# Performance work log

Hardware: AMD Instinct MI355X
Metric: run time of the kernel (lower is better)

Reference implementation:

```python
import jax, jax.numpy as jnp
import numpy as np
import math

N, D, F = 8192, 512, 2048
M, K = 4096, 128  # masked cells, masked genes per cell
EPS = 1e-5


def setup_inputs() -> dict:
    key = jax.random.key(0)
    ks = jax.random.split(key, 16)
    s = 0.02
    x = jax.random.normal(ks[0], (N, D), jnp.float32)
    # distinct masked cell indices (torch.randperm semantics)
    mask_nodes = jax.random.permutation(ks[1], N)[:M].astype(jnp.int64)
    # per-row distinct gene indices (torch.randperm per row)
    gene_idx = jnp.argsort(jax.random.uniform(ks[2], (M, D)), axis=1)[:, :K].astype(jnp.int64)
    return {
        'x': x, 'mask_nodes': mask_nodes, 'gene_idx': gene_idx,
        'Wq_e': s * jax.random.normal(ks[3], (D, D), jnp.float32),
        'Wk_e': s * jax.random.normal(ks[4], (D, D), jnp.float32),
        'Wv_e': s * jax.random.normal(ks[5], (D, D), jnp.float32),
        'ln1_g': jnp.ones((D,), jnp.float32), 'ln1_b': jnp.zeros((D,), jnp.float32),
        'ff_W1': s * jax.random.normal(ks[6], (D, F), jnp.float32),
        'ff_b1': jnp.zeros((F,), jnp.float32),
        'ff_W2': s * jax.random.normal(ks[7], (F, D), jnp.float32),
        'ff_b2': jnp.zeros((D,), jnp.float32),
        'ln2_g': jnp.ones((D,), jnp.float32), 'ln2_b': jnp.zeros((D,), jnp.float32),
        'Wq_d': s * jax.random.normal(ks[8], (D, D), jnp.float32),
        'Wk_d': s * jax.random.normal(ks[9], (D, D), jnp.float32),
        'Wv_d': s * jax.random.normal(ks[10], (D, D), jnp.float32),
        'ln3_g': jnp.ones((D,), jnp.float32), 'ln3_b': jnp.zeros((D,), jnp.float32),
        'ln4_g': jnp.ones((D,), jnp.float32), 'ln4_b': jnp.zeros((D,), jnp.float32),
        'head_W': s * jax.random.normal(ks[11], (D, D), jnp.float32),
        'head_b': jnp.zeros((D,), jnp.float32),
    }


def _ln(h, g, b):
    mu = jnp.mean(h, axis=-1, keepdims=True)
    var = jnp.mean(jnp.square(h - mu), axis=-1, keepdims=True)
    return (h - mu) * jax.lax.rsqrt(var + EPS) * g + b


def _attn(h, Wq, Wk, Wv):
    Q = h @ Wq
    Kt = h @ Wk
    V = h @ Wv
    scores = (Q @ Kt.T) / math.sqrt(D)  # [N, N]
    attn = jax.nn.softmax(scores, axis=-1)
    return attn @ V, attn


def _ff(h, W1, b1, W2, b2):
    return jax.nn.gelu(h @ W1 + b1, approximate=False) @ W2 + b2


def reference(x, mask_nodes, gene_idx,
              Wq_e, Wk_e, Wv_e, ln1_g, ln1_b,
              ff_W1, ff_b1, ff_W2, ff_b2, ln2_g, ln2_b,
              Wq_d, Wk_d, Wv_d, ln3_g, ln3_b, ln4_g, ln4_b,
              head_W, head_b):
    # mask selected genes of selected cells to 0 (encoding_mask_nodes)
    rows = mask_nodes[:, None]
    use_x = x.at[rows, gene_idx].set(0.0)

    hidden, encode_weights = _attn(use_x, Wq_e, Wk_e, Wv_e)
    hidden = _ln(hidden + use_x, ln1_g, ln1_b)
    hidden = _ln(hidden + _ff(hidden, ff_W1, ff_b1, ff_W2, ff_b2), ln2_g, ln2_b)
    # NOTE: `hidden[mask_nodes][gene_mask] = 0` in the original torch code
    # writes into a copy produced by advanced indexing -> it is a no-op.

    recon, _ = _attn(hidden, Wq_d, Wk_d, Wv_d)
    recon = _ln(recon + hidden, ln3_g, ln3_b)
    # original reuses self.ff (not self.ff1) in the decoder block
    recon = _ln(recon + _ff(recon, ff_W1, ff_b1, ff_W2, ff_b2), ln4_g, ln4_b)
    h = recon @ head_W + head_b

    x_init = x[rows, gene_idx]      # [M, K]
    x_recon = h[rows, gene_idx]     # [M, K]
    return (x_init, x_recon, encode_weights, recon)
```

## Files before the change

kernel.cpp:

```cpp
#include <hip/hip_runtime.h>
#include <hip/hip_bf16.h>
#include <stdint.h>
#include <math.h>

typedef __bf16 bf16_t;
typedef __bf16 bf16x8 __attribute__((ext_vector_type(8)));
typedef __bf16 bf16x4 __attribute__((ext_vector_type(4)));
typedef float floatx4 __attribute__((ext_vector_type(4)));

#define NN 8192
#define DD 512
#define FF 2048
#define MM 4096
#define KK 128

template<typename T> struct V16;
template<> struct V16<bf16_t> { using t = bf16x8;  static const int sh = 3; };
template<> struct V16<float>  { using t = floatx4; static const int sh = 2; };

__device__ __forceinline__ void async_copy16(const void* g, void* l) {
    __builtin_amdgcn_global_load_lds(
        (const __attribute__((address_space(1))) void*)(uintptr_t)g,
        (__attribute__((address_space(3))) void*)(uint32_t)(uintptr_t)l,
        16, 0, 0);
}

template<int EPI, typename OT>
__global__ __launch_bounds__(256, 3)
void gemm_nt(const bf16_t* __restrict__ A, const bf16_t* __restrict__ B,
             OT* __restrict__ C,
             int M, int Nc, int Kd, int ldA, int ldB, int ldC,
             long partStride, float scale, const float* __restrict__ bias,
             float* __restrict__ denom)
{
    __shared__ char smem[32768];
    bf16_t* As0 = (bf16_t*)smem;
    bf16_t* As1 = As0 + 4096;
    bf16_t* Bs0 = As0 + 8192;
    bf16_t* Bs1 = As0 + 12288;

    const int tid  = threadIdx.x;
    const int lane = tid & 63;
    const int wave = tid >> 6;
    const int wm   = (wave >> 1) << 6;
    const int wn   = (wave & 1) << 6;
    const int quad = lane >> 4;
    const int l16  = lane & 15;

    const int gx   = gridDim.x;
    const int nwg  = gx * gridDim.y;
    const int orig = blockIdx.y * gx + blockIdx.x;
    const int swz  = (orig & 7) * (nwg >> 3) + (orig >> 3);
    const long bm  = (long)(swz % gx) * 128;
    const long bn  = (long)(swz / gx) * 128;

    const int  kchunk = Kd / gridDim.z;
    const long kBeg   = (long)blockIdx.z * kchunk;
    OT* __restrict__ Co = C + (long)blockIdx.z * partStride;

    const int t0 = tid, t1 = tid + 256;
    const int r0 = t0 >> 2, q0 = (t0 & 3) ^ (r0 & 3) ^ ((r0 >> 2) & 3);
    const int r1 = t1 >> 2, q1 = (t1 & 3) ^ (r1 & 3) ^ ((r1 >> 2) & 3);
    const bf16_t* pA0 = A + (bm + r0) * (long)ldA + q0 * 8 + kBeg;
    const bf16_t* pA1 = A + (bm + r1) * (long)ldA + q1 * 8 + kBeg;
    const bf16_t* pB0 = B + (bn + r0) * (long)ldB + q0 * 8 + kBeg;
    const bf16_t* pB1 = B + (bn + r1) * (long)ldB + q1 * 8 + kBeg;

    floatx4 acc[4][4] = {};

    auto stage = [&](bf16_t* Ab, bf16_t* Bb, long k0) {
        async_copy16(pA0 + k0, Ab + t0 * 8);
        async_copy16(pA1 + k0, Ab + t1 * 8);
        async_copy16(pB0 + k0, Bb + t0 * 8);
        async_copy16(pB1 + k0, Bb + t1 * 8);
    };
    const int csw = (l16 & 3) ^ (l16 >> 2);
    auto compute = [&](const bf16_t* Ab, const bf16_t* Bb) {
        bf16x8 af[4], bfr[4];
#pragma unroll
        for (int i = 0; i < 4; i++) {
            af[i]  = *(const bf16x8*)&Ab[(wm + i * 16 + l16) * 32 + (quad ^ csw) * 8];
            bfr[i] = *(const bf16x8*)&Bb[(wn + i * 16 + l16) * 32 + (quad ^ csw) * 8];
        }
#pragma unroll
        for (int mi = 0; mi < 4; mi++)
#pragma unroll
            for (int ni = 0; ni < 4; ni++)
                acc[mi][ni] = __builtin_amdgcn_mfma_f32_16x16x32_bf16(
                    af[mi], bfr[ni], acc[mi][ni], 0, 0, 0);
    };

    const int nt = kchunk >> 5;
    stage(As0, Bs0, 0);
    __syncthreads();
    long kk = 32;
    for (int t = 0; t < nt; t += 2) {
        stage(As1, Bs1, kk); kk += 32;
        compute(As0, Bs0);
        __syncthreads();
        if (t + 2 < nt) { stage(As0, Bs0, kk); kk += 32; }
        compute(As1, Bs1);
        __syncthreads();
    }

    OT* sm = (OT*)smem;
    const int g = wm >> 6;
#pragma unroll
    for (int mi = 0; mi < 4; mi++) {
        if (mi) __syncthreads();
        const long rbase = bm + wm + mi * 16 + quad * 4;
        if (EPI == 4) {
#pragma unroll
            for (int r = 0; r < 4; r++) {
                float rsum = 0.0f;
#pragma unroll
                for (int ni = 0; ni < 4; ni++) {
                    float v = __expf(acc[mi][ni][r] * scale);
                    rsum += v;
                    sm[(g * 16 + quad * 4 + r) * 128 + wn + ni * 16 + l16] = (OT)v;
                }
                rsum += __shfl_xor(rsum, 1);
                rsum += __shfl_xor(rsum, 2);
                rsum += __shfl_xor(rsum, 4);
                rsum += __shfl_xor(rsum, 8);
                if (l16 == 0) atomicAdd(denom + rbase + r, rsum);
            }
        } else {
#pragma unroll
            for (int ni = 0; ni < 4; ni++) {
                float bv = (EPI >= 2) ? bias[bn + wn + ni * 16 + l16] : 0.0f;
#pragma unroll
                for (int r = 0; r < 4; r++) {
                    float v = acc[mi][ni][r];
                    if (EPI == 1) v *= scale;
                    if (EPI >= 2) v += bv;
                    if (EPI == 3) v = 0.5f * v * (1.0f + erff(v * 0.70710678118f));
                    sm[(g * 16 + quad * 4 + r) * 128 + wn + ni * 16 + l16] = (OT)v;
                }
            }
        }
        __syncthreads();
        typedef typename V16<OT>::t VT;
        const int VSH = V16<OT>::sh;
        const int VEC = 1 << VSH;
        const int NP  = (32 * 128) / (256 * VEC);
#pragma unroll
        for (int p = 0; p < NP; p++) {
            const int vid  = p * 256 + tid;
            const int lrow = vid >> (7 - VSH);
            const int vcol = vid & ((128 >> VSH) - 1);
            const long grow = bm + (lrow >> 4) * 64 + mi * 16 + (lrow & 15);
            *(VT*)&Co[grow * (long)ldC + bn + vcol * VEC] =
                *(const VT*)&sm[lrow * 128 + vcol * VEC];
        }
    }
}

template<int EPI, typename OT>
static void launch_gemm(const bf16_t* A, const bf16_t* B, OT* C,
                        int M, int Nc, int Kd, int lda, int ldb, int ldc,
                        int splitk, long partStride, float scale,
                        const float* bias, float* denom, hipStream_t s)
{
    dim3 g(M / 128, Nc / 128, splitk);
    gemm_nt<EPI, OT><<<g, 256, 0, s>>>(A, B, C, M, Nc, Kd, lda, ldb, ldc,
                                       partStride, scale, bias, denom);
}

__global__ __launch_bounds__(256)
void transpose_f2b(const float* __restrict__ in, bf16_t* __restrict__ out,
                   int R, int C)
{
    __shared__ float tile[32][33];
    const int bx = blockIdx.x * 32;
    const int by = blockIdx.y * 32;
    const int tx = threadIdx.x, ty = threadIdx.y;
#pragma unroll
    for (int i = 0; i < 32; i += 8)
        tile[ty + i][tx] = in[(long)(by + ty + i) * C + bx + tx];
    __syncthreads();
#pragma unroll
    for (int i = 0; i < 32; i += 8)
        out[(long)(bx + ty + i) * R + by + tx] = (bf16_t)tile[tx][ty + i];
}

__global__ __launch_bounds__(256)
void transpose_b2b(const bf16_t* __restrict__ in, bf16_t* __restrict__ out,
                   int R, int C, int ldin)
{
    __shared__ bf16_t tile[32][34];
    const int bx = blockIdx.x * 32;
    const int by = blockIdx.y * 32;
    const int tx = threadIdx.x, ty = threadIdx.y;
#pragma unroll
    for (int i = 0; i < 32; i += 8)
        tile[ty + i][tx] = in[(long)(by + ty + i) * ldin + bx + tx];
    __syncthreads();
#pragma unroll
    for (int i = 0; i < 32; i += 8)
        out[(long)(bx + ty + i) * R + by + tx] = tile[tx][ty + i];
}

__global__ __launch_bounds__(256)
void encw_norm(const bf16_t* __restrict__ P, const float* __restrict__ denom,
               float* __restrict__ out)
{
    const long row = blockIdx.x;
    const float inv = 1.0f / denom[row];
    const bf16_t* p = P + row * (long)NN;
    float* q = out + row * (long)NN;
    const int tid = threadIdx.x;
#pragma unroll
    for (int i = 0; i < 4; i++) {
        const int o = (tid + i * 256) * 8;
        bf16x8 v = *(const bf16x8*)(p + o);
        float4 lo, hi;
        lo.x = (float)v[0] * inv; lo.y = (float)v[1] * inv;
        lo.z = (float)v[2] * inv; lo.w = (float)v[3] * inv;
        hi.x = (float)v[4] * inv; hi.y = (float)v[5] * inv;
        hi.z = (float)v[6] * inv; hi.w = (float)v[7] * inv;
        *(float4*)(q + o)     = lo;
        *(float4*)(q + o + 4) = hi;
    }
}

__global__ __launch_bounds__(256)
void zero_f32(float* __restrict__ p)
{
    p[blockIdx.x * 256 + threadIdx.x] = 0.0f;
}

template<int NP, bool RS, bool CB>
__global__ __launch_bounds__(64)
void add_ln_gen(const float* __restrict__ a, long pstride,
                const float* __restrict__ rs, const float* __restrict__ cb,
                const float* __restrict__ b,
                const float* __restrict__ g, const float* __restrict__ be,
                bf16_t* __restrict__ ob, float* __restrict__ of)
{
    const long row = blockIdx.x;
    const int lane = threadIdx.x;
    const long base = row * DD + lane * 8;
    const float irs = RS ? (1.0f / rs[row]) : 1.0f;
    float v[8], s = 0.0f, s2 = 0.0f;
#pragma unroll
    for (int j = 0; j < 8; j++) {
        float t = 0.0f;
#pragma unroll
        for (int p = 0; p < NP; p++) t += a[base + j + p * pstride];
        t *= irs;
        if (CB) t += cb[lane * 8 + j];
        t += b[base + j];
        v[j] = t;
        s += t; s2 += t * t;
    }
#pragma unroll
    for (int off = 32; off > 0; off >>= 1) {
        s  += __shfl_xor(s,  off);
        s2 += __shfl_xor(s2, off);
    }
    const float mu  = s * (1.0f / DD);
    const float var = s2 * (1.0f / DD) - mu * mu;
    const float inv = rsqrtf(var + 1e-5f);
    bf16x8 o;
#pragma unroll
    for (int j = 0; j < 8; j++) {
        float r = (v[j] - mu) * inv * g[lane * 8 + j] + be[lane * 8 + j];
        o[j] = (bf16_t)r;
        of[base + j] = r;
    }
    *(bf16x8*)(ob + base) = o;
}

__global__ __launch_bounds__(256)
void build_usex(const float* __restrict__ x, bf16_t* __restrict__ ub,
                float* __restrict__ uf)
{
    const long i = ((long)blockIdx.x * 256 + threadIdx.x) * 4;
    const float4 v = *(const float4*)(x + i);
    *(float4*)(uf + i) = v;
    bf16x4 o = { (bf16_t)v.x, (bf16_t)v.y, (bf16_t)v.z, (bf16_t)v.w };
    *(bf16x4*)(ub + i) = o;
}

__global__ __launch_bounds__(256)
void scatter_zero(bf16_t* __restrict__ ub, float* __restrict__ uf,
                  const int* __restrict__ mn, const int* __restrict__ gi)
{
    const int i = blockIdx.x * 256 + threadIdx.x;
    const long idx = (long)mn[i >> 7] * DD + gi[i];
    ub[idx] = (bf16_t)0.0f;
    uf[idx] = 0.0f;
}

__global__ __launch_bounds__(256)
void gather_mk(const float* __restrict__ src, const int* __restrict__ mn,
               const int* __restrict__ gi, float* __restrict__ dst)
{
    const int i = blockIdx.x * 256 + threadIdx.x;
    dst[i] = src[(long)mn[i >> 7] * DD + gi[i]];
}

__global__ __launch_bounds__(256)
void gather_head(const float* __restrict__ p1, long pstride,
                 const float* __restrict__ hb, const int* __restrict__ mn,
                 const int* __restrict__ gi, float* __restrict__ dst)
{
    const int i = blockIdx.x * 256 + threadIdx.x;
    const int col = gi[i];
    const long idx = (long)mn[i >> 7] * DD + col;
    dst[i] = p1[idx] + p1[idx + pstride] + hb[col];
}

extern "C" void kernel_launch(void* const* d_in, const int* in_sizes, int n_in,
                              void* d_out, int out_size, void* d_ws, size_t ws_size,
                              hipStream_t stream)
{
    const float* x      = (const float*)d_in[0];
    const int*   mn     = (const int*)d_in[1];
    const int*   gi     = (const int*)d_in[2];
    const float* Wq_e   = (const float*)d_in[3];
    const float* Wk_e   = (const float*)d_in[4];
    const float* Wv_e   = (const float*)d_in[5];
    const float* ln1_g  = (const float*)d_in[6];
    const float* ln1_b  = (const float*)d_in[7];
    const float* ff_W1  = (const float*)d_in[8];
    const float* ff_b1  = (const float*)d_in[9];
    const float* ff_W2  = (const float*)d_in[10];
    const float* ff_b2  = (const float*)d_in[11];
    const float* ln2_g  = (const float*)d_in[12];
    const float* ln2_b  = (const float*)d_in[13];
    const float* Wq_d   = (const float*)d_in[14];
    const float* Wk_d   = (const float*)d_in[15];
    const float* Wv_d   = (const float*)d_in[16];
    const float* ln3_g  = (const float*)d_in[17];
    const float* ln3_b  = (const float*)d_in[18];
    const float* ln4_g  = (const float*)d_in[19];
    const float* ln4_b  = (const float*)d_in[20];
    const float* head_W = (const float*)d_in[21];
    const float* head_b = (const float*)d_in[22];

    float* outf     = (float*)d_out;
    float* o_xinit  = outf;
    float* o_xrecon = outf + (size_t)MM * KK;
    float* o_encw   = outf + (size_t)2 * MM * KK;
    float* o_recon  = o_encw + (size_t)NN * NN;

    char* ws = (char*)d_ws;
    size_t off = 0;
    auto alloc = [&](size_t bytes) -> void* {
        void* p = ws + off;
        off += (bytes + 255) & ~(size_t)255;
        return p;
    };
    const size_t NDb = (size_t)NN * DD * sizeof(bf16_t);
    const size_t NDf = (size_t)NN * DD * sizeof(float);
    const long   NDe = (long)NN * DD;

    bf16_t* usex_b = (bf16_t*)alloc(NDb);
    bf16_t* qkv_b  = (bf16_t*)alloc((size_t)NN * 3 * DD * 2);
    bf16_t* vt_b   = (bf16_t*)alloc(NDb);
    bf16_t* hid_b  = (bf16_t*)alloc(NDb);
    float*  usex_f = (float*)alloc(NDf);
    float*  resA_f = (float*)alloc(NDf);
    float*  part_f = (float*)alloc(2 * NDf);
    bf16_t* wt_qe  = (bf16_t*)alloc((size_t)DD * DD * 2);
    bf16_t* wt_ke  = (bf16_t*)alloc((size_t)DD * DD * 2);
    bf16_t* wt_ve  = (bf16_t*)alloc((size_t)DD * DD * 2);
    bf16_t* wt_qd  = (bf16_t*)alloc((size_t)DD * DD * 2);
    bf16_t* wt_kd  = (bf16_t*)alloc((size_t)DD * DD * 2);
    bf16_t* wt_vd  = (bf16_t*)alloc((size_t)DD * DD * 2);
    bf16_t* wt_h   = (bf16_t*)alloc((size_t)DD * DD * 2);
    bf16_t* w1t    = (bf16_t*)alloc((size_t)DD * FF * 2);
    bf16_t* w2t    = (bf16_t*)alloc((size_t)FF * DD * 2);
    float*  denom  = (float*)alloc((size_t)NN * sizeof(float));
    bf16_t* scores = (bf16_t*)alloc((size_t)NN * NN * 2);
    bf16_t* t1_b   = scores;
    float*  resB_f = usex_f;
    (void)ws_size; (void)in_sizes; (void)n_in; (void)out_size;
    (void)wt_ke; (void)wt_ve; (void)wt_kd; (void)wt_vd;

    auto tr = [&](const float* in, bf16_t* o, int R, int C) {
        transpose_f2b<<<dim3(C / 32, R / 32), dim3(32, 8), 0, stream>>>(in, o, R, C);
    };
    const float SC = 0.04419417382f;

    tr(Wq_e, wt_qe, DD, DD);  tr(Wk_e, wt_ke, DD, DD);  tr(Wv_e, wt_ve, DD, DD);
    tr(Wq_d, wt_qd, DD, DD);  tr(Wk_d, wt_kd, DD, DD);  tr(Wv_d, wt_vd, DD, DD);
    tr(head_W, wt_h, DD, DD); tr(ff_W1, w1t, DD, FF);   tr(ff_W2, w2t, FF, DD);

    build_usex<<<NN * DD / 1024, 256, 0, stream>>>(x, usex_b, usex_f);
    scatter_zero<<<MM * KK / 256, 256, 0, stream>>>(usex_b, usex_f, mn, gi);
    gather_mk<<<MM * KK / 256, 256, 0, stream>>>(x, mn, gi, o_xinit);

    launch_gemm<0, bf16_t>(usex_b, wt_qe, qkv_b,
                           NN, 3 * DD, DD, DD, DD, 3 * DD, 1, 0, 0.f, nullptr,
                           nullptr, stream);
    transpose_b2b<<<dim3(DD / 32, NN / 32), dim3(32, 8), 0, stream>>>(
        qkv_b + 2 * DD, vt_b, NN, DD, 3 * DD);
    zero_f32<<<NN / 256, 256, 0, stream>>>(denom);
    launch_gemm<4, bf16_t>(qkv_b, qkv_b + DD, scores,
                           NN, NN, DD, 3 * DD, 3 * DD, NN, 1, 0, SC, nullptr,
                           denom, stream);
    encw_norm<<<NN, 256, 0, stream>>>(scores, denom, o_encw);
    launch_gemm<0, float>(scores, vt_b, part_f,
                          NN, DD, NN, NN, NN, DD, 2, NDe, 0.f, nullptr,
                          nullptr, stream);
    add_ln_gen<2, true, false><<<NN, 64, 0, stream>>>(
        part_f, NDe, denom, nullptr, usex_f, ln1_g, ln1_b, hid_b, resA_f);

    launch_gemm<3, bf16_t>(hid_b, w1t, t1_b,
                           NN, FF, DD, DD, DD, FF, 1, 0, 0.f, ff_b1,
                           nullptr, stream);
    launch_gemm<0, float>(t1_b, w2t, part_f,
                          NN, DD, FF, FF, FF, DD, 2, NDe, 0.f, nullptr,
                          nullptr, stream);
    add_ln_gen<2, false, true><<<NN, 64, 0, stream>>>(
        part_f, NDe, nullptr, ff_b2, resA_f, ln2_g, ln2_b, hid_b, resB_f);

    launch_gemm<0, bf16_t>(hid_b, wt_qd, qkv_b,
                           NN, 3 * DD, DD, DD, DD, 3 * DD, 1, 0, 0.f, nullptr,
                           nullptr, stream);
    transpose_b2b<<<dim3(DD / 32, NN / 32), dim3(32, 8), 0, stream>>>(
        qkv_b + 2 * DD, vt_b, NN, DD, 3 * DD);
    zero_f32<<<NN / 256, 256, 0, stream>>>(denom);
    launch_gemm<4, bf16_t>(qkv_b, qkv_b + DD, scores,
                           NN, NN, DD, 3 * DD, 3 * DD, NN, 1, 0, SC, nullptr,
                           denom, stream);
    launch_gemm<0, float>(scores, vt_b, part_f,
                          NN, DD, NN, NN, NN, DD, 2, NDe, 0.f, nullptr,
                          nullptr, stream);
    add_ln_gen<2, true, false><<<NN, 64, 0, stream>>>(
        part_f, NDe, denom, nullptr, resB_f, ln3_g, ln3_b, hid_b, resA_f);

    launch_gemm<3, bf16_t>(hid_b, w1t, t1_b,
                           NN, FF, DD, DD, DD, FF, 1, 0, 0.f, ff_b1,
                           nullptr, stream);
    launch_gemm<0, float>(t1_b, w2t, part_f,
                          NN, DD, FF, FF, FF, DD, 2, NDe, 0.f, nullptr,
                          nullptr, stream);
    add_ln_gen<2, false, true><<<NN, 64, 0, stream>>>(
        part_f, NDe, nullptr, ff_b2, resA_f, ln4_g, ln4_b, hid_b, o_recon);

    launch_gemm<0, float>(hid_b, wt_h, part_f,
                          NN, DD, DD, DD, DD, DD, 2, NDe, 0.f, nullptr,
                          nullptr, stream);
    gather_head<<<MM * KK / 256, 256, 0, stream>>>(part_f, NDe, head_b,
                                                   mn, gi, o_xrecon);
}
```

Before: 1.095 ms.

## Triple-buffer GEMM K-loop and compute head only for masked rows

The GEMM main loop moves from double buffering with full syncthreads to a three-stage LDS ring. Explicit vmcnt waits and raw s_barrier calls let two tiles stay in flight while one is being computed. Separately, the final head projection now runs only on the masked-cell rows: those rows are gathered into a compact buffer, which halves that GEMM. The larger LDS footprint (48KB) may lower occupancy at launch_bounds 3, and the hand-written waitcnt counts assume exactly four loads per stage.

```diff
diff --git a/kernel.cpp b/kernel.cpp
--- a/kernel.cpp
+++ b/kernel.cpp
@@ -33,11 +33,9 @@
              long partStride, float scale, const float* __restrict__ bias,
              float* __restrict__ denom)
 {
-    __shared__ char smem[32768];
-    bf16_t* As0 = (bf16_t*)smem;
-    bf16_t* As1 = As0 + 4096;
-    bf16_t* Bs0 = As0 + 8192;
-    bf16_t* Bs1 = As0 + 12288;
+    __shared__ char smem[49152];
+    bf16_t* Abase = (bf16_t*)smem;
+    bf16_t* Bbase = Abase + 12288;
 
     const int tid  = threadIdx.x;
     const int lane = tid & 63;
@@ -68,14 +66,18 @@
 
     floatx4 acc[4][4] = {};
 
-    auto stage = [&](bf16_t* Ab, bf16_t* Bb, long k0) {
+    auto stage = [&](int buf, long k0) {
+        bf16_t* Ab = Abase + buf * 4096;
+        bf16_t* Bb = Bbase + buf * 4096;
         async_copy16(pA0 + k0, Ab + t0 * 8);
         async_copy16(pA1 + k0, Ab + t1 * 8);
         async_copy16(pB0 + k0, Bb + t0 * 8);
         async_copy16(pB1 + k0, Bb + t1 * 8);
     };
     const int csw = (l16 & 3) ^ (l16 >> 2);
-    auto compute = [&](const bf16_t* Ab, const bf16_t* Bb) {
+    auto compute = [&](int buf) {
+        const bf16_t* Ab = Abase + buf * 4096;
+        const bf16_t* Bb = Bbase + buf * 4096;
         bf16x8 af[4], bfr[4];
 #pragma unroll
         for (int i = 0; i < 4; i++) {
@@ -91,16 +93,24 @@
     };
 
     const int nt = kchunk >> 5;
-    stage(As0, Bs0, 0);
-    __syncthreads();
-    long kk = 32;
-    for (int t = 0; t < nt; t += 2) {
-        stage(As1, Bs1, kk); kk += 32;
-        compute(As0, Bs0);
-        __syncthreads();
-        if (t + 2 < nt) { stage(As0, Bs0, kk); kk += 32; }
-        compute(As1, Bs1);
-        __syncthreads();
+    stage(0, 0);
+    stage(1, 32);
+    long kk = 64;
+    for (int t = 0; t < nt; ++t) {
+        const int cur = t % 3;
+        if (t + 2 < nt) {
+            stage((t + 2) % 3, kk); kk += 32;
+            asm volatile("s_waitcnt vmcnt(8)" ::: "memory");
+        } else if (t + 1 < nt) {
+            asm volatile("s_waitcnt vmcnt(4)" ::: "memory");
+        } else {
+            asm volatile("s_waitcnt vmcnt(0)" ::: "memory");
+        }
+        __builtin_amdgcn_s_barrier();
+        __builtin_amdgcn_sched_barrier(0);
+        compute(cur);
+        __builtin_amdgcn_sched_barrier(0);
+        __builtin_amdgcn_s_barrier();
     }
 
     OT* sm = (OT*)smem;
@@ -301,14 +311,24 @@
     dst[i] = src[(long)mn[i >> 7] * DD + gi[i]];
 }
 
+__global__ __launch_bounds__(64)
+void gather_rows(const bf16_t* __restrict__ src, const int* __restrict__ mn,
+                 bf16_t* __restrict__ dst)
+{
+    const long r = blockIdx.x;
+    const long s = (long)mn[r] * DD;
+    const int t = threadIdx.x;
+    *(bf16x8*)(dst + r * DD + t * 8) = *(const bf16x8*)(src + s + t * 8);
+}
+
 __global__ __launch_bounds__(256)
 void gather_head(const float* __restrict__ p1, long pstride,
-                 const float* __restrict__ hb, const int* __restrict__ mn,
-                 const int* __restrict__ gi, float* __restrict__ dst)
+                 const float* __restrict__ hb, const int* __restrict__ gi,
+                 float* __restrict__ dst)
 {
     const int i = blockIdx.x * 256 + threadIdx.x;
     const int col = gi[i];
-    const long idx = (long)mn[i >> 7] * DD + col;
+    const long idx = (long)(i >> 7) * DD + col;
     dst[i] = p1[idx] + p1[idx + pstride] + hb[col];
 }
 
@@ -356,6 +376,7 @@
     const size_t NDb = (size_t)NN * DD * sizeof(bf16_t);
     const size_t NDf = (size_t)NN * DD * sizeof(float);
     const long   NDe = (long)NN * DD;
+    const long   MDe = (long)MM * DD;
 
     bf16_t* usex_b = (bf16_t*)alloc(NDb);
     bf16_t* qkv_b  = (bf16_t*)alloc((size_t)NN * 3 * DD * 2);
@@ -373,6 +394,7 @@
     bf16_t* wt_h   = (bf16_t*)alloc((size_t)DD * DD * 2);
     bf16_t* w1t    = (bf16_t*)alloc((size_t)DD * FF * 2);
     bf16_t* w2t    = (bf16_t*)alloc((size_t)FF * DD * 2);
+    bf16_t* hcomp  = (bf16_t*)alloc((size_t)MM * DD * 2);
     float*  denom  = (float*)alloc((size_t)NN * sizeof(float));
     bf16_t* scores = (bf16_t*)alloc((size_t)NN * NN * 2);
     bf16_t* t1_b   = scores;
@@ -442,9 +464,10 @@
     add_ln_gen<2, false, true><<<NN, 64, 0, stream>>>(
         part_f, NDe, nullptr, ff_b2, resA_f, ln4_g, ln4_b, hid_b, o_recon);
 
-    launch_gemm<0, float>(hid_b, wt_h, part_f,
-                          NN, DD, DD, DD, DD, DD, 2, NDe, 0.f, nullptr,
+    gather_rows<<<MM, 64, 0, stream>>>(hid_b, mn, hcomp);
+    launch_gemm<0, float>(hcomp, wt_h, part_f,
+                          MM, DD, DD, DD, DD, DD, 2, MDe, 0.f, nullptr,
                           nullptr, stream);
-    gather_head<<<MM * KK / 256, 256, 0, stream>>>(part_f, NDe, head_b,
-                                                   mn, gi, o_xrecon);
-}
+    gather_head<<<MM * KK / 256, 256, 0, stream>>>(part_f, MDe, head_b,
+                                                   gi, o_xrecon);
+}
```

New measurement: 1.105 ms. Within noise of the previous version (+0.9%).
